# Kernel optimization log

Hardware: AMD Instinct MI355X
Metric: run time of the kernel (lower is better)

## Reference

```python
import jax, jax.numpy as jnp
import numpy as np


def setup_inputs() -> dict:
    key = jax.random.key(0)
    ks = jax.random.split(key, 7)
    B, S, D, KP = 16, 4096, 64, 256  # batch*heads, seq_len, head_dim, linformer proj dim
    Q = jax.random.normal(ks[0], (B, S, D), dtype=jnp.float32)
    K = jax.random.normal(ks[1], (B, S, D), dtype=jnp.float32)
    V = jax.random.normal(ks[2], (B, S, D), dtype=jnp.float32)
    E_w = jax.random.normal(ks[3], (KP, S), dtype=jnp.float32) / np.sqrt(S)
    E_b = jax.random.normal(ks[4], (KP,), dtype=jnp.float32) * 0.01
    F_w = jax.random.normal(ks[5], (KP, S), dtype=jnp.float32) / np.sqrt(S)
    F_b = jax.random.normal(ks[6], (KP,), dtype=jnp.float32) * 0.01
    return {"Q": Q, "K": K, "V": V, "E_w": E_w, "E_b": E_b, "F_w": F_w, "F_b": F_b}


def reference(Q, K, V, E_w, E_b, F_w, F_b):
    # Linformer head (mask=None path); dropout is identity at inference.
    dim_k = K.shape[-1]
    scale = 1.0 / jnp.sqrt(jnp.float32(dim_k))
    # K.permute(0,2,1) -> [B, d, S]; E projects seq axis S -> k: [B, d, k]
    Kp = jnp.einsum('bsd,ks->bdk', K, E_w) + E_b  # [B, d, k]
    # V.permute -> F -> permute back: [B, k, d]
    Vp = jnp.einsum('bsd,ks->bkd', V, F_w) + F_b[None, :, None]  # [B, k, d]
    scores = jnp.einsum('bsd,bdk->bsk', Q, Kp) * scale  # [B, S, k]
    attn = jax.nn.softmax(scores, axis=-1)
    out = jnp.einsum('bsk,bkd->bsd', attn, Vp)  # [B, S, d]
    return (out, attn)
```

## Files before the change

kernel.cpp:

```cpp
#include <hip/hip_runtime.h>


#define B_  16
#define S_  4096
#define D_  64
#define KP_ 256

typedef short v8s __attribute__((ext_vector_type(8)));
typedef float v4f __attribute__((ext_vector_type(4)));

__device__ __forceinline__ short f2bf(float x) {
    union { float f; unsigned u; } v; v.f = x;
    unsigned r = v.u + 0x7FFFu + ((v.u >> 16) & 1u);
    return (short)(r >> 16);
}
__device__ __forceinline__ float bf2f(short h) {
    union { float f; unsigned u; } v; v.u = ((unsigned)(unsigned short)h) << 16;
    return v.f;
}

__global__ __launch_bounds__(256)
void wcvt_kernel(const float* __restrict__ E_w, const float* __restrict__ F_w,
                 short* __restrict__ Whi, short* __restrict__ Wlo)
{
    const int p = blockIdx.y;
    const float* W = p ? F_w : E_w;
    const size_t i4 = (size_t)blockIdx.x * 256 + threadIdx.x;
    float4 v = ((const float4*)W)[i4];
    short4 h, lo;
    h.x = f2bf(v.x); lo.x = f2bf(v.x - bf2f(h.x));
    h.y = f2bf(v.y); lo.y = f2bf(v.y - bf2f(h.y));
    h.z = f2bf(v.z); lo.z = f2bf(v.z - bf2f(h.z));
    h.w = f2bf(v.w); lo.w = f2bf(v.w - bf2f(h.w));
    const size_t o = (size_t)p * (KP_ * S_) + i4 * 4;
    *(short4*)(Whi + o) = h;
    *(short4*)(Wlo + o) = lo;
}

__global__ __launch_bounds__(512, 2)
void proj_mfma_kernel(const float* __restrict__ Kg, const float* __restrict__ Vg,
                      const short* __restrict__ Whi, const short* __restrict__ Wlo,
                      float* __restrict__ PpartK, float* __restrict__ PpartV)
{
    const int sc = blockIdx.x;
    const int p  = blockIdx.y;
    const int b  = blockIdx.z;

    const float* src = (p ? Vg : Kg) + ((size_t)b * S_ + sc * 512) * D_;
    const short* Wh = Whi + (size_t)p * KP_ * S_ + sc * 512;
    const short* Wl = Wlo + (size_t)p * KP_ * S_ + sc * 512;

    __shared__ __align__(16) short Af[2][2][4][512];

    const int t  = threadIdx.x;
    const int wv = t >> 6;
    const int l  = t & 63;

    v4f acc[2][4];
#pragma unroll
    for (int i = 0; i < 2; ++i)
#pragma unroll
        for (int m = 0; m < 4; ++m) acc[i][m] = (v4f){0.f, 0.f, 0.f, 0.f};

    const bool do_stage = (t < 256);
    const int sd   = t & 63;
    const int soct = (t >> 6) & 3;
    const int smt  = sd >> 4;
    const int sfl  = (sd & 15) + soct * 16;

    float g[8];
    if (do_stage) {
        const float* sp = src + (size_t)(soct * 8) * D_ + sd;
#pragma unroll
        for (int j = 0; j < 8; ++j) g[j] = sp[(size_t)j * D_];
        v8s hi, lo;
#pragma unroll
        for (int j = 0; j < 8; ++j) { short h = f2bf(g[j]); hi[j] = h; lo[j] = f2bf(g[j] - bf2f(h)); }
        *(v8s*)&Af[0][0][smt][sfl * 8] = hi;
        *(v8s*)&Af[0][1][smt][sfl * 8] = lo;
    }
    __syncthreads();

    const int krow0 = wv * 32;

    for (int st = 0; st < 16; ++st) {
        const int cur = st & 1;
        if (st + 1 < 16 && do_stage) {
            const float* sp = src + (size_t)((st + 1) * 32 + soct * 8) * D_ + sd;
#pragma unroll
            for (int j = 0; j < 8; ++j) g[j] = sp[(size_t)j * D_];
        }
        v8s wh[2], wl2[2];
#pragma unroll
        for (int i = 0; i < 2; ++i) {
            size_t off = (size_t)(krow0 + i * 16 + (l & 15)) * S_ + st * 32 + (l >> 4) * 8;
            wh[i]  = *(const v8s*)(Wh + off);
            wl2[i] = *(const v8s*)(Wl + off);
        }
        v8s sh[4], sl[4];
#pragma unroll
        for (int m = 0; m < 4; ++m) {
            sh[m] = *(const v8s*)&Af[cur][0][m][l * 8];
            sl[m] = *(const v8s*)&Af[cur][1][m][l * 8];
        }
        if (p == 0) {
#pragma unroll
            for (int i = 0; i < 2; ++i)
#pragma unroll
                for (int m = 0; m < 4; ++m) {
                    acc[i][m] = __builtin_amdgcn_mfma_f32_16x16x32_bf16(wh[i],  sh[m], acc[i][m], 0, 0, 0);
                    acc[i][m] = __builtin_amdgcn_mfma_f32_16x16x32_bf16(wh[i],  sl[m], acc[i][m], 0, 0, 0);
                    acc[i][m] = __builtin_amdgcn_mfma_f32_16x16x32_bf16(wl2[i], sh[m], acc[i][m], 0, 0, 0);
                }
        } else {
#pragma unroll
            for (int i = 0; i < 2; ++i)
#pragma unroll
                for (int m = 0; m < 4; ++m) {
                    acc[i][m] = __builtin_amdgcn_mfma_f32_16x16x32_bf16(sh[m], wh[i],  acc[i][m], 0, 0, 0);
                    acc[i][m] = __builtin_amdgcn_mfma_f32_16x16x32_bf16(sl[m], wh[i],  acc[i][m], 0, 0, 0);
                    acc[i][m] = __builtin_amdgcn_mfma_f32_16x16x32_bf16(sh[m], wl2[i], acc[i][m], 0, 0, 0);
                }
        }
        if (st + 1 < 16 && do_stage) {
            v8s hi, lo;
#pragma unroll
            for (int j = 0; j < 8; ++j) { short h = f2bf(g[j]); hi[j] = h; lo[j] = f2bf(g[j] - bf2f(h)); }
            *(v8s*)&Af[cur ^ 1][0][smt][sfl * 8] = hi;
            *(v8s*)&Af[cur ^ 1][1][smt][sfl * 8] = lo;
        }
        __syncthreads();
    }

    if (p == 0) {
        float* outp = PpartK + ((size_t)sc * B_ + b) * (KP_ * D_);
#pragma unroll
        for (int i = 0; i < 2; ++i)
#pragma unroll
            for (int m = 0; m < 4; ++m)
#pragma unroll
                for (int r = 0; r < 4; ++r) {
                    int k = krow0 + i * 16 + (l >> 4) * 4 + r;
                    int d = m * 16 + (l & 15);
                    outp[(size_t)k * D_ + d] = acc[i][m][r];
                }
    } else {
        float* outp = PpartV + ((size_t)sc * B_ + b) * (KP_ * D_);
#pragma unroll
        for (int i = 0; i < 2; ++i)
#pragma unroll
            for (int m = 0; m < 4; ++m)
#pragma unroll
                for (int r = 0; r < 4; ++r) {
                    int d = m * 16 + (l >> 4) * 4 + r;
                    int k = krow0 + i * 16 + (l & 15);
                    outp[(size_t)d * KP_ + k] = acc[i][m][r];
                }
    }
}

__global__ __launch_bounds__(256)
void reduce_kernel(const float* __restrict__ PpartK, const float* __restrict__ PpartV,
                   const float* __restrict__ E_b, const float* __restrict__ F_b,
                   short* __restrict__ Kp_hi, short* __restrict__ Kp_lo,
                   short* __restrict__ Vp_hi)
{
    const int j    = blockIdx.x * 256 + threadIdx.x;
    const int side = j >> 16;
    const int i4   = j & 65535;
    const int flat = i4 * 4;
    const int b    = flat >> 14;
    const int dk   = flat & 16383;

    if (side == 0) {
        float4 a = make_float4(0.f, 0.f, 0.f, 0.f);
#pragma unroll
        for (int sc = 0; sc < 8; ++sc) {
            float4 v = *(const float4*)(PpartK + ((size_t)sc * B_ + b) * (KP_ * D_) + dk);
            a.x += v.x; a.y += v.y; a.z += v.z; a.w += v.w;
        }
        const int k = dk >> 6, d = dk & 63;
        float be = E_b[k];
        a.x += be; a.y += be; a.z += be; a.w += be;
        short4 h, lo;
        h.x = f2bf(a.x); lo.x = f2bf(a.x - bf2f(h.x));
        h.y = f2bf(a.y); lo.y = f2bf(a.y - bf2f(h.y));
        h.z = f2bf(a.z); lo.z = f2bf(a.z - bf2f(h.z));
        h.w = f2bf(a.w); lo.w = f2bf(a.w - bf2f(h.w));
        const size_t fo = (((size_t)b * 2 + (d >> 5)) * 16 + (k >> 4)) * 512
                        + (size_t)((k & 15) + ((d >> 3) & 3) * 16) * 8 + (d & 7);
        *(short4*)(Kp_hi + fo) = h;
        *(short4*)(Kp_lo + fo) = lo;
    } else {
        float4 a = make_float4(0.f, 0.f, 0.f, 0.f);
#pragma unroll
        for (int sc = 0; sc < 8; ++sc) {
            float4 v = *(const float4*)(PpartV + ((size_t)sc * B_ + b) * (KP_ * D_) + dk);
            a.x += v.x; a.y += v.y; a.z += v.z; a.w += v.w;
        }
        const int d = dk >> 8, k = dk & 255;
        float4 bf = *(const float4*)(F_b + k);
        a.x += bf.x; a.y += bf.y; a.z += bf.z; a.w += bf.w;
        short4 h;
        h.x = f2bf(a.x); h.y = f2bf(a.y); h.z = f2bf(a.z); h.w = f2bf(a.w);
        const size_t fo = (((size_t)b * 8 + (k >> 5)) * 4 + (d >> 4)) * 512
                        + (size_t)((d & 15) + ((k >> 3) & 3) * 16) * 8 + (k & 7);
        *(short4*)(Vp_hi + fo) = h;
    }
}

__global__ __launch_bounds__(256, 3)
void attn_mfma_kernel(const float* __restrict__ Qg,
                      const short* __restrict__ Kp_hi, const short* __restrict__ Kp_lo,
                      const short* __restrict__ Vp_hi,
                      float* __restrict__ attn_out, float* __restrict__ outg)
{
    const int st = blockIdx.x;
    const int b  = blockIdx.y;
    const int t  = threadIdx.x;
    const int wv = t >> 6;
    const int l  = t & 63;

    __shared__ __align__(16) short smem[64 * 264];
    __shared__ __align__(16) float Fst[4][4][264];
    short (*Qf)[2][4][512] = (short (*)[2][4][512])smem;
    short* Pl  = smem;
    short* KLl = smem + 8192;
    short* KLh = (short*)&Fst[0][0][0];

    {
        const int s    = t & 63;
        const int doct = t >> 6;
        const float* qrow = Qg + ((size_t)b * S_ + st * 64 + s) * D_;
        const int mt = s >> 4, fl = (s & 15) + doct * 16;
#pragma unroll
        for (int kd = 0; kd < 2; ++kd) {
            float4 v0 = *(const float4*)(qrow + kd * 32 + doct * 8);
            float4 v1 = *(const float4*)(qrow + kd * 32 + doct * 8 + 4);
            float gq[8] = {v0.x, v0.y, v0.z, v0.w, v1.x, v1.y, v1.z, v1.w};
            v8s hi, lo;
#pragma unroll
            for (int jj = 0; jj < 8; ++jj) { short h = f2bf(gq[jj]); hi[jj] = h; lo[jj] = f2bf(gq[jj] - bf2f(h)); }
            *(v8s*)&Qf[kd][0][mt][fl * 8] = hi;
            *(v8s*)&Qf[kd][1][mt][fl * 8] = lo;
        }
    }
    __syncthreads();

    v4f acc2[16];
#pragma unroll
    for (int nt = 0; nt < 16; ++nt) acc2[nt] = (v4f){0.f, 0.f, 0.f, 0.f};
#pragma unroll
    for (int kd = 0; kd < 2; ++kd) {
        {
            const size_t tbl = (((size_t)b * 2 + kd) * 16) * 512;
            const int4* gh = (const int4*)(Kp_hi + tbl);
            const int4* gl = (const int4*)(Kp_lo + tbl);
            int4* lh = (int4*)KLh;
            int4* ll = (int4*)KLl;
#pragma unroll
            for (int i = 0; i < 4; ++i) lh[t + i * 256] = gh[t + i * 256];
#pragma unroll
            for (int i = 0; i < 4; ++i) ll[t + i * 256] = gl[t + i * 256];
        }
        __syncthreads();
        v8s Ah = *(const v8s*)&Qf[kd][0][wv][l * 8];
        v8s Al = *(const v8s*)&Qf[kd][1][wv][l * 8];
#pragma unroll
        for (int nt = 0; nt < 16; ++nt) {
            v8s Bh = *(const v8s*)&KLh[nt * 512 + l * 8];
            v8s Bl = *(const v8s*)&KLl[nt * 512 + l * 8];
            acc2[nt] = __builtin_amdgcn_mfma_f32_16x16x32_bf16(Ah, Bh, acc2[nt], 0, 0, 0);
            acc2[nt] = __builtin_amdgcn_mfma_f32_16x16x32_bf16(Al, Bh, acc2[nt], 0, 0, 0);
            acc2[nt] = __builtin_amdgcn_mfma_f32_16x16x32_bf16(Ah, Bl, acc2[nt], 0, 0, 0);
        }
        __syncthreads();
    }

    const float scale = 0.125f;
    float* attn_b = attn_out + ((size_t)b * S_ + st * 64) * KP_;
    const int g = l >> 4;
#pragma unroll
    for (int r = 0; r < 4; ++r) {
        float m = -3.4e38f;
#pragma unroll
        for (int nt = 0; nt < 16; ++nt) m = fmaxf(m, acc2[nt][r]);
        m = fmaxf(m, __shfl_xor(m, 1));
        m = fmaxf(m, __shfl_xor(m, 2));
        m = fmaxf(m, __shfl_xor(m, 4));
        m = fmaxf(m, __shfl_xor(m, 8));
        float sum = 0.f;
#pragma unroll
        for (int nt = 0; nt < 16; ++nt) {
            float e = __expf((acc2[nt][r] - m) * scale);
            acc2[nt][r] = e; sum += e;
        }
        sum += __shfl_xor(sum, 1);
        sum += __shfl_xor(sum, 2);
        sum += __shfl_xor(sum, 4);
        sum += __shfl_xor(sum, 8);
        const float inv = 1.f / sum;
        const int s_loc = wv * 16 + g * 4 + r;
#pragma unroll
        for (int nt = 0; nt < 16; ++nt) {
            float pv = acc2[nt][r] * inv;
            Fst[wv][g][nt * 16 + (l & 15)] = pv;
            Pl[s_loc * 264 + nt * 16 + (l & 15)] = f2bf(pv);
        }
#pragma unroll
        for (int gg = 0; gg < 4; ++gg) {
            float4 vv = *(const float4*)&Fst[wv][gg][l * 4];
            *(float4*)(attn_b + (size_t)(wv * 16 + gg * 4 + r) * KP_ + l * 4) = vv;
        }
    }
    __syncthreads();
    {
        const int4* gv = (const int4*)(Vp_hi + (size_t)b * 16384);
        int4* lv = (int4*)KLh;
#pragma unroll
        for (int i = 0; i < 4; ++i) lv[t + i * 256] = gv[t + i * 256];
    }
    __syncthreads();
    v4f acc3[4];
#pragma unroll
    for (int nt = 0; nt < 4; ++nt) acc3[nt] = (v4f){0.f, 0.f, 0.f, 0.f};
#pragma unroll
    for (int kc = 0; kc < 8; ++kc) {
        v8s A3 = *(const v8s*)&Pl[(wv * 16 + (l & 15)) * 264 + kc * 32 + (l >> 4) * 8];
#pragma unroll
        for (int nt = 0; nt < 4; ++nt) {
            v8s B3 = (kc < 4)
                ? *(const v8s*)&KLh[(kc * 4 + nt) * 512 + l * 8]
                : *(const v8s*)(Vp_hi + (((size_t)b * 8 + kc) * 4 + nt) * 512 + (size_t)l * 8);
            acc3[nt] = __builtin_amdgcn_mfma_f32_16x16x32_bf16(A3, B3, acc3[nt], 0, 0, 0);
        }
    }
    float* out_b = outg + ((size_t)b * S_ + st * 64) * D_;
#pragma unroll
    for (int nt = 0; nt < 4; ++nt)
#pragma unroll
        for (int r = 0; r < 4; ++r) {
            int s_loc = wv * 16 + (l >> 4) * 4 + r;
            out_b[(size_t)s_loc * D_ + nt * 16 + (l & 15)] = acc3[nt][r];
        }
}

extern "C" void kernel_launch(void* const* d_in, const int* in_sizes, int n_in,
                              void* d_out, int out_size, void* d_ws, size_t ws_size,
                              hipStream_t stream) {
    const float* Q   = (const float*)d_in[0];
    const float* K   = (const float*)d_in[1];
    const float* V   = (const float*)d_in[2];
    const float* E_w = (const float*)d_in[3];
    const float* E_b = (const float*)d_in[4];
    const float* F_w = (const float*)d_in[5];
    const float* F_b = (const float*)d_in[6];

    float* out  = (float*)d_out;
    float* attn = out + (size_t)B_ * S_ * D_;

    short* Whi   = (short*)d_ws;
    short* Wlo   = Whi + (size_t)2 * KP_ * S_;
    short* Kp_hi = Wlo + (size_t)2 * KP_ * S_;
    short* Kp_lo = Kp_hi + (size_t)B_ * KP_ * D_;
    short* Vp_hi = Kp_lo + (size_t)B_ * KP_ * D_;

    float* PpartK = attn;
    float* PpartV = attn + (size_t)8 * B_ * KP_ * D_;

    wcvt_kernel<<<dim3(KP_ * S_ / 4 / 256, 2), 256, 0, stream>>>(E_w, F_w, Whi, Wlo);
    proj_mfma_kernel<<<dim3(8, 2, B_), 512, 0, stream>>>(K, V, Whi, Wlo, PpartK, PpartV);
    reduce_kernel<<<dim3(512), 256, 0, stream>>>(PpartK, PpartV, E_b, F_b, Kp_hi, Kp_lo, Vp_hi);
    attn_mfma_kernel<<<dim3(S_ / 64, B_), 256, 0, stream>>>(Q, Kp_hi, Kp_lo, Vp_hi, attn, out);
}
```

Baseline: 183.8 us.

## Pre-swizzle projection weights into MFMA fragments, prefetch them, stage second Vp half via LDS

The weight conversion kernel now writes the bf16 hi/lo E/F weights in a fragment-ordered layout, so each lane's 16-byte load in the projection kernel is contiguous and coalesced instead of strided by the sequence length. The projection loop becomes a two-step ping-pong that prefetches the next step's weight fragments into registers while the current MFMAs run. In the attention-output kernel, the second half of Vp is copied into shared memory in a second pass instead of being read directly from global memory inside the MFMA loop. These changes trade extra registers and an additional barrier pair for better coalescing and more load/compute overlap.

Measured after the change: 181.2 us (median of 2 runs). About the same (-1.4%).

```diff
diff --git a/kernel.cpp b/kernel.cpp
--- a/kernel.cpp
+++ b/kernel.cpp
@@ -32,9 +32,12 @@
     h.y = f2bf(v.y); lo.y = f2bf(v.y - bf2f(h.y));
     h.z = f2bf(v.z); lo.z = f2bf(v.z - bf2f(h.z));
     h.w = f2bf(v.w); lo.w = f2bf(v.w - bf2f(h.w));
-    const size_t o = (size_t)p * (KP_ * S_) + i4 * 4;
-    *(short4*)(Whi + o) = h;
-    *(short4*)(Wlo + o) = lo;
+    const int k  = (int)(i4 >> 10);
+    const int s0 = (int)(i4 & 1023) << 2;
+    const size_t fo = (((size_t)p * 16 + (k >> 4)) * 128 + (s0 >> 5)) * 512
+                    + (size_t)(((k & 15) + ((s0 >> 3) & 3) * 16) * 8) + (s0 & 7);
+    *(short4*)(Whi + fo) = h;
+    *(short4*)(Wlo + fo) = lo;
 }
 
 __global__ __launch_bounds__(512, 2)
@@ -47,14 +50,15 @@
     const int b  = blockIdx.z;
 
     const float* src = (p ? Vg : Kg) + ((size_t)b * S_ + sc * 512) * D_;
-    const short* Wh = Whi + (size_t)p * KP_ * S_ + sc * 512;
-    const short* Wl = Wlo + (size_t)p * KP_ * S_ + sc * 512;
 
     __shared__ __align__(16) short Af[2][2][4][512];
 
     const int t  = threadIdx.x;
     const int wv = t >> 6;
     const int l  = t & 63;
+    const int k16 = wv * 2;
+
+    const size_t wbase = ((size_t)p * 16 + k16) * 128 * 512 + (size_t)(sc * 16) * 512 + (size_t)l * 8;
 
     v4f acc[2][4];
 #pragma unroll
@@ -68,6 +72,14 @@
     const int smt  = sd >> 4;
     const int sfl  = (sd & 15) + soct * 16;
 
+    v8s whA[2], wlA[2], whB[2], wlB[2];
+#pragma unroll
+    for (int i = 0; i < 2; ++i) {
+        size_t o = wbase + (size_t)i * 65536;
+        whA[i] = *(const v8s*)(Whi + o);
+        wlA[i] = *(const v8s*)(Wlo + o);
+    }
+
     float g[8];
     if (do_stage) {
         const float* sp = src + (size_t)(soct * 8) * D_ + sd;
@@ -81,21 +93,20 @@
     }
     __syncthreads();
 
-    const int krow0 = wv * 32;
-
-    for (int st = 0; st < 16; ++st) {
+    auto step = [&](int st, v8s (&whc)[2], v8s (&wlc)[2], v8s (&whn)[2], v8s (&wln)[2]) {
         const int cur = st & 1;
-        if (st + 1 < 16 && do_stage) {
-            const float* sp = src + (size_t)((st + 1) * 32 + soct * 8) * D_ + sd;
-#pragma unroll
-            for (int j = 0; j < 8; ++j) g[j] = sp[(size_t)j * D_];
-        }
-        v8s wh[2], wl2[2];
-#pragma unroll
-        for (int i = 0; i < 2; ++i) {
-            size_t off = (size_t)(krow0 + i * 16 + (l & 15)) * S_ + st * 32 + (l >> 4) * 8;
-            wh[i]  = *(const v8s*)(Wh + off);
-            wl2[i] = *(const v8s*)(Wl + off);
+        if (st + 1 < 16) {
+#pragma unroll
+            for (int i = 0; i < 2; ++i) {
+                size_t o = wbase + (size_t)i * 65536 + (size_t)(st + 1) * 512;
+                whn[i] = *(const v8s*)(Whi + o);
+                wln[i] = *(const v8s*)(Wlo + o);
+            }
+            if (do_stage) {
+                const float* sp = src + (size_t)((st + 1) * 32 + soct * 8) * D_ + sd;
+#pragma unroll
+                for (int j = 0; j < 8; ++j) g[j] = sp[(size_t)j * D_];
+            }
         }
         v8s sh[4], sl[4];
 #pragma unroll
@@ -108,18 +119,18 @@
             for (int i = 0; i < 2; ++i)
 #pragma unroll
                 for (int m = 0; m < 4; ++m) {
-                    acc[i][m] = __builtin_amdgcn_mfma_f32_16x16x32_bf16(wh[i],  sh[m], acc[i][m], 0, 0, 0);
-                    acc[i][m] = __builtin_amdgcn_mfma_f32_16x16x32_bf16(wh[i],  sl[m], acc[i][m], 0, 0, 0);
-                    acc[i][m] = __builtin_amdgcn_mfma_f32_16x16x32_bf16(wl2[i], sh[m], acc[i][m], 0, 0, 0);
+                    acc[i][m] = __builtin_amdgcn_mfma_f32_16x16x32_bf16(whc[i], sh[m], acc[i][m], 0, 0, 0);
+                    acc[i][m] = __builtin_amdgcn_mfma_f32_16x16x32_bf16(whc[i], sl[m], acc[i][m], 0, 0, 0);
+                    acc[i][m] = __builtin_amdgcn_mfma_f32_16x16x32_bf16(wlc[i], sh[m], acc[i][m], 0, 0, 0);
                 }
         } else {
 #pragma unroll
             for (int i = 0; i < 2; ++i)
 #pragma unroll
                 for (int m = 0; m < 4; ++m) {
-                    acc[i][m] = __builtin_amdgcn_mfma_f32_16x16x32_bf16(sh[m], wh[i],  acc[i][m], 0, 0, 0);
-                    acc[i][m] = __builtin_amdgcn_mfma_f32_16x16x32_bf16(sl[m], wh[i],  acc[i][m], 0, 0, 0);
-                    acc[i][m] = __builtin_amdgcn_mfma_f32_16x16x32_bf16(sh[m], wl2[i], acc[i][m], 0, 0, 0);
+                    acc[i][m] = __builtin_amdgcn_mfma_f32_16x16x32_bf16(sh[m], whc[i], acc[i][m], 0, 0, 0);
+                    acc[i][m] = __builtin_amdgcn_mfma_f32_16x16x32_bf16(sl[m], whc[i], acc[i][m], 0, 0, 0);
+                    acc[i][m] = __builtin_amdgcn_mfma_f32_16x16x32_bf16(sh[m], wlc[i], acc[i][m], 0, 0, 0);
                 }
         }
         if (st + 1 < 16 && do_stage) {
@@ -130,8 +141,14 @@
             *(v8s*)&Af[cur ^ 1][1][smt][sfl * 8] = lo;
         }
         __syncthreads();
-    }
-
+    };
+
+    for (int st2 = 0; st2 < 16; st2 += 2) {
+        step(st2,     whA, wlA, whB, wlB);
+        step(st2 + 1, whB, wlB, whA, wlA);
+    }
+
+    const int krow0 = wv * 32;
     if (p == 0) {
         float* outp = PpartK + ((size_t)sc * B_ + b) * (KP_ * D_);
 #pragma unroll
@@ -325,13 +342,28 @@
 #pragma unroll
     for (int nt = 0; nt < 4; ++nt) acc3[nt] = (v4f){0.f, 0.f, 0.f, 0.f};
 #pragma unroll
-    for (int kc = 0; kc < 8; ++kc) {
+    for (int kc = 0; kc < 4; ++kc) {
         v8s A3 = *(const v8s*)&Pl[(wv * 16 + (l & 15)) * 264 + kc * 32 + (l >> 4) * 8];
 #pragma unroll
         for (int nt = 0; nt < 4; ++nt) {
-            v8s B3 = (kc < 4)
-                ? *(const v8s*)&KLh[(kc * 4 + nt) * 512 + l * 8]
-                : *(const v8s*)(Vp_hi + (((size_t)b * 8 + kc) * 4 + nt) * 512 + (size_t)l * 8);
+            v8s B3 = *(const v8s*)&KLh[(kc * 4 + nt) * 512 + l * 8];
+            acc3[nt] = __builtin_amdgcn_mfma_f32_16x16x32_bf16(A3, B3, acc3[nt], 0, 0, 0);
+        }
+    }
+    __syncthreads();
+    {
+        const int4* gv = (const int4*)(Vp_hi + (size_t)b * 16384 + 8192);
+        int4* lv = (int4*)KLh;
+#pragma unroll
+        for (int i = 0; i < 4; ++i) lv[t + i * 256] = gv[t + i * 256];
+    }
+    __syncthreads();
+#pragma unroll
+    for (int kc = 4; kc < 8; ++kc) {
+        v8s A3 = *(const v8s*)&Pl[(wv * 16 + (l & 15)) * 264 + kc * 32 + (l >> 4) * 8];
+#pragma unroll
+        for (int nt = 0; nt < 4; ++nt) {
+            v8s B3 = *(const v8s*)&KLh[((kc - 4) * 4 + nt) * 512 + l * 8];
             acc3[nt] = __builtin_amdgcn_mfma_f32_16x16x32_bf16(A3, B3, acc3[nt], 0, 0, 0);
         }
     }
```
